# Kernel optimization log

Hardware: AMD Instinct MI355X
Metric: run time of the kernel (lower is better)

Reference implementation:

```python
import jax, jax.numpy as jnp
import numpy as np


def setup_inputs() -> dict:
    key = jax.random.key(0)
    k1, k2 = jax.random.split(key)
    N, D, n_bags, per_bag = 8192, 512, 64, 128
    features = jax.random.normal(k1, (N, D), dtype=jnp.float32)
    # sorted bag indicator: 64 bags x 128 instances each
    batch = jnp.repeat(jnp.arange(n_bags, dtype=jnp.int32), per_bag)
    W = jax.random.normal(k2, (D, D), dtype=jnp.float32) * np.float32(1.0 / np.sqrt(D))
    b = jnp.zeros((D,), dtype=jnp.float32)
    return {"features": features, "W": W, "b": b, "batch": batch, "n_topk": 16, "n_bags": n_bags}


def reference(features, W, b, batch, n_topk, n_bags):
    N = features.shape[0]
    # F.normalize(dim=1): x / max(||x||, eps)
    norm = jnp.sqrt(jnp.sum(features * features, axis=1, keepdims=True))
    nf = features / jnp.maximum(norm, 1e-12)
    corr = nf @ nf.T  # [N, N] cosine-similarity map
    same_bag = batch[:, None] == batch[None, :]
    adj = jnp.where(same_bag, corr, 0.0)
    # scatter-zero the (N - n_topk) smallest per row == keep n_topk largest per row
    _, top_idx = jax.lax.top_k(adj, n_topk)  # [N, n_topk]
    keep = jnp.zeros((N, N), dtype=bool).at[jnp.arange(N)[:, None], top_idx].set(True)
    adj = jnp.where(keep, adj, 0.0)
    # dense_to_sparse()[0] keeps only indices -> unit edge weights for GCNConv.
    # GCNConv (gcn_norm, add_self_loops=True): A_hat = binarized adjacency with diag forced to 1.
    eye = jnp.eye(N, dtype=bool)
    A = jnp.where(eye, 1.0, (adj != 0).astype(features.dtype))  # [N, N]
    deg = jnp.sum(A, axis=0)  # degree scattered on target (col) index in PyG
    dis = jax.lax.rsqrt(deg)  # deg >= 1 thanks to self loops
    xw = features @ W  # [N, D]
    # out[col] = d[col]^-1/2 * sum_row A[row,col] * d[row]^-1/2 * xw[row]
    gcn_out = dis[:, None] * (A.T @ (dis[:, None] * xw)) + b
    # one-hot^T @ features == per-bag segment sum
    agg = jax.ops.segment_sum(gcn_out, batch, num_segments=n_bags)  # [n_bags, D]
    return agg, adj
```

## Files before the change

kernel.cpp:

```cpp
#include <hip/hip_runtime.h>
#include <hip/hip_bf16.h>

#define N 8192
#define D 512
#define NBAGS 64
#define PER_BAG 128
#define TOPK 16

typedef float vfloat4 __attribute__((ext_vector_type(4)));

#define WS_INVN   0
#define WS_KIDX   32768
#define WS_KCNT   557056
#define WS_DEG    589824
#define WS_FW     622592

__global__ void norm_kernel(const float* __restrict__ feat,
                            float* __restrict__ invn,
                            int* __restrict__ deg) {
    int t = threadIdx.x;
    if (blockIdx.x < 32) deg[blockIdx.x * 256 + t] = 0;
    int lane = t & 63, w = t >> 6;
    int r = blockIdx.x * 4 + w;
    const float4* fr = (const float4*)(feat + (size_t)r * D);
    float4 a = fr[lane];
    float4 bq = fr[lane + 64];
    float ss = a.x * a.x + a.y * a.y + a.z * a.z + a.w * a.w
             + bq.x * bq.x + bq.y * bq.y + bq.z * bq.z + bq.w * bq.w;
    #pragma unroll
    for (int off = 32; off > 0; off >>= 1) ss += __shfl_down(ss, off);
    if (lane == 0) invn[r] = 1.0f / fmaxf(sqrtf(ss), 1e-12f);
}

__global__ __launch_bounds__(256, 4) void simtopk_kernel(
        const float* __restrict__ feat,
        const float* __restrict__ invn,
        float* __restrict__ adjOut,
        int* __restrict__ keptIdx,
        int* __restrict__ keptCnt,
        int* __restrict__ deg) {
    int rg = blockIdx.x;
    int bag = blockIdx.y;
    int t = threadIdx.x;
    __shared__ float colT[2][32][132];
    __shared__ float rowT[2][32][12];
    int bagBase = bag * PER_BAG;
    int rowBase = bagBase + rg * 8;
    int tx = t & 31;
    int ty = t >> 5;
    float4 acc = make_float4(0.f, 0.f, 0.f, 0.f);

    int kk = t & 31;
    int sub = t >> 5;
    int winHalf = bag >> 5;
    int jw = (bag & 31) >> 3;
    int winLo = (bag & 31) * 32, winHi = winLo + 32;
    vfloat4 zf4 = {0.f, 0.f, 0.f, 0.f};

    #pragma unroll
    for (int c0 = 0; c0 < 16; ++c0)
        colT[0][kk][sub * 16 + c0] =
            feat[(size_t)(bagBase + sub * 16 + c0) * D + kk];
    rowT[0][kk][sub] = feat[(size_t)(rowBase + sub) * D + kk];
    __syncthreads();

    float pf[16], pr;
    for (int it = 0; it < 16; ++it) {
        int cur = it & 1;
        if (it < 15) {
            int k0 = (it + 1) * 32;
            #pragma unroll
            for (int c0 = 0; c0 < 16; ++c0)
                pf[c0] = feat[(size_t)(bagBase + sub * 16 + c0) * D + k0 + kk];
            pr = feat[(size_t)(rowBase + sub) * D + k0 + kk];
        }
        {
            int zr = it >> 1, half = it & 1;
            vfloat4* rowp = (vfloat4*)(adjOut + (size_t)(rowBase + zr) * N)
                            + half * 1024;
            bool hasWin = (half == winHalf);
            #pragma unroll
            for (int j = 0; j < 4; ++j) {
                int f = t + 256 * j;
                if (hasWin && j == jw) {
                    if (f < winLo || f >= winHi)
                        __builtin_nontemporal_store(zf4, &rowp[f]);
                } else {
                    __builtin_nontemporal_store(zf4, &rowp[f]);
                }
            }
        }
        #pragma unroll
        for (int k = 0; k < 32; ++k) {
            float4 cv = *(const float4*)&colT[cur][k][4 * tx];
            float rv = rowT[cur][k][ty];
            acc.x += rv * cv.x; acc.y += rv * cv.y;
            acc.z += rv * cv.z; acc.w += rv * cv.w;
        }
        if (it < 15) {
            int nxt = cur ^ 1;
            #pragma unroll
            for (int c0 = 0; c0 < 16; ++c0)
                colT[nxt][kk][sub * 16 + c0] = pf[c0];
            rowT[nxt][kk][sub] = pr;
        }
        __syncthreads();
    }
    float ic0 = invn[bagBase + 4 * tx];
    float ic1 = invn[bagBase + 4 * tx + 1];
    float ic2 = invn[bagBase + 4 * tx + 2];
    float ic3 = invn[bagBase + 4 * tx + 3];
    float ir = invn[rowBase + ty];
    acc.x *= ir * ic0; acc.y *= ir * ic1;
    acc.z *= ir * ic2; acc.w *= ir * ic3;

    {
        int r = rowBase + ty;
        float o0 = acc.x, o1 = acc.y, o2 = acc.z, o3 = acc.w;
        float w0 = o0, w1 = o1, w2 = o2, w3 = o3;
        int pm = 0, cnt = 0;
        #pragma unroll 1
        for (int itk = 0; itk < TOPK; ++itk) {
            float bv = w0; int bj = 0;
            if (w1 > bv) { bv = w1; bj = 1; }
            if (w2 > bv) { bv = w2; bj = 2; }
            if (w3 > bv) { bv = w3; bj = 3; }
            int bi = 4 * tx + bj;
            #pragma unroll
            for (int s = 1; s < 32; s <<= 1) {
                float ov = __shfl_xor(bv, s);
                int oi = __shfl_xor(bi, s);
                if (ov > bv || (ov == bv && oi < bi)) { bv = ov; bi = oi; }
            }
            if (bv <= 0.0f) break;
            if (tx == 0) keptIdx[(size_t)r * TOPK + cnt] = bi;
            cnt++;
            if ((bi >> 2) == tx) {
                pm |= 1 << (bi & 3);
                int q = bi & 3;
                if (q == 0) w0 = -1e30f;
                else if (q == 1) w1 = -1e30f;
                else if (q == 2) w2 = -1e30f;
                else w3 = -1e30f;
            }
        }
        if (tx == 0) keptCnt[r] = cnt;
        float4 ov4 = make_float4((pm & 1) ? o0 : 0.0f,
                                 (pm & 2) ? o1 : 0.0f,
                                 (pm & 4) ? o2 : 0.0f,
                                 (pm & 8) ? o3 : 0.0f);
        *(float4*)(adjOut + (size_t)r * N + bagBase + 4 * tx) = ov4;
        if (pm & 1) atomicAdd(&deg[bagBase + 4 * tx], 1);
        if (pm & 2) atomicAdd(&deg[bagBase + 4 * tx + 1], 1);
        if (pm & 4) atomicAdd(&deg[bagBase + 4 * tx + 2], 1);
        if (pm & 8) atomicAdd(&deg[bagBase + 4 * tx + 3], 1);
        int selfCol = rg * 8 + ty;
        if (tx == (selfCol >> 2) && !((pm >> (selfCol & 3)) & 1))
            atomicAdd(&deg[bagBase + selfCol], 1);
    }
}

__global__ void wfw_kernel(const float* __restrict__ feat,
                           const int* __restrict__ keptIdx,
                           const int* __restrict__ keptCnt,
                           const int* __restrict__ deg,
                           float* __restrict__ FW) {
    int bag = blockIdx.x;
    int chunk = blockIdx.y;
    int t = threadIdx.x;
    __shared__ float wsh[PER_BAG];
    int bagBase = bag * PER_BAG;
    {
        int r = bagBase + t;
        int cnt = keptCnt[r];
        float sum = 0.0f;
        bool selfin = false;
        for (int k = 0; k < cnt; ++k) {
            int c = keptIdx[(size_t)r * TOPK + k];
            if (c == t) selfin = true;
            sum += rsqrtf((float)deg[bagBase + c]);
        }
        float disr = rsqrtf((float)deg[r]);
        if (!selfin) sum += disr;
        wsh[t] = disr * sum;
    }
    __syncthreads();
    int d = chunk * 128 + t;
    float acc = 0.0f;
    #pragma unroll 8
    for (int r = 0; r < PER_BAG; ++r)
        acc += wsh[r] * feat[(size_t)(bagBase + r) * D + d];
    FW[bag * D + d] = acc;
}

__global__ void agg_kernel(const float* __restrict__ FW,
                           const float* __restrict__ Wm,
                           const float* __restrict__ b,
                           float* __restrict__ aggOut) {
    int bag = blockIdx.x;
    int chunk = blockIdx.y;
    int t = threadIdx.x;
    __shared__ float fws[D];
    fws[t] = FW[bag * D + t];
    fws[256 + t] = FW[bag * D + 256 + t];
    __syncthreads();
    int d = chunk * 256 + t;
    float acc = 0.0f;
    #pragma unroll 8
    for (int k = 0; k < D; ++k)
        acc += fws[k] * Wm[(size_t)k * D + d];
    aggOut[bag * D + d] = acc + 128.0f * b[d];
}

extern "C" void kernel_launch(void* const* d_in, const int* in_sizes, int n_in,
                              void* d_out, int out_size, void* d_ws, size_t ws_size,
                              hipStream_t stream) {
    const float* feat = (const float*)d_in[0];
    const float* Wm   = (const float*)d_in[1];
    const float* b    = (const float*)d_in[2];

    char* ws = (char*)d_ws;
    float* invn   = (float*)(ws + WS_INVN);
    int* keptIdx  = (int*)(ws + WS_KIDX);
    int* keptCnt  = (int*)(ws + WS_KCNT);
    int* deg      = (int*)(ws + WS_DEG);
    float* FW     = (float*)(ws + WS_FW);

    float* aggOut = (float*)d_out;
    float* adjOut = (float*)d_out + NBAGS * D;

    norm_kernel<<<N / 4, 256, 0, stream>>>(feat, invn, deg);
    simtopk_kernel<<<dim3(16, NBAGS), 256, 0, stream>>>(feat, invn, adjOut,
                                                        keptIdx, keptCnt, deg);
    wfw_kernel<<<dim3(NBAGS, 4), PER_BAG, 0, stream>>>(feat, keptIdx, keptCnt,
                                                       deg, FW);
    agg_kernel<<<dim3(NBAGS, 2), 256, 0, stream>>>(FW, Wm, b, aggOut);
}
```

Baseline: 346.4 us.

## Compute 4 rows per thread in similarity-topk kernel to reuse column tiles

Each block of the similarity/top-k kernel now handles 32 rows of a bag instead of 8. Each thread computes a 4x4 register tile, so every column tile loaded from LDS is reused across four rows, and LDS writes are vectorised to float4. The grid shrinks from 16x64 to 4x64 blocks, which cuts redundant global loads of the bag's column features. In exchange, each block zero-fills four times more of the dense adjacency output, and the lower block count with launch bounds of 1 may reduce occupancy and latency hiding on the store-bound zero-fill.

```diff
diff --git a/kernel.cpp b/kernel.cpp
--- a/kernel.cpp
+++ b/kernel.cpp
@@ -32,7 +32,7 @@
     if (lane == 0) invn[r] = 1.0f / fmaxf(sqrtf(ss), 1e-12f);
 }
 
-__global__ __launch_bounds__(256, 4) void simtopk_kernel(
+__global__ __launch_bounds__(256, 1) void simtopk_kernel(
         const float* __restrict__ feat,
         const float* __restrict__ invn,
         float* __restrict__ adjOut,
@@ -43,28 +43,32 @@
     int bag = blockIdx.y;
     int t = threadIdx.x;
     __shared__ float colT[2][32][132];
-    __shared__ float rowT[2][32][12];
+    __shared__ float rowT[2][32][36];
     int bagBase = bag * PER_BAG;
-    int rowBase = bagBase + rg * 8;
+    int rowBase = bagBase + rg * 32;
     int tx = t & 31;
     int ty = t >> 5;
-    float4 acc = make_float4(0.f, 0.f, 0.f, 0.f);
-
     int kk = t & 31;
     int sub = t >> 5;
-    int winHalf = bag >> 5;
-    int jw = (bag & 31) >> 3;
-    int winLo = (bag & 31) * 32, winHi = winLo + 32;
-    vfloat4 zf4 = {0.f, 0.f, 0.f, 0.f};
+
+    float4 acc[4];
+    #pragma unroll
+    for (int rr = 0; rr < 4; ++rr) acc[rr] = make_float4(0.f, 0.f, 0.f, 0.f);
 
     #pragma unroll
     for (int c0 = 0; c0 < 16; ++c0)
         colT[0][kk][sub * 16 + c0] =
             feat[(size_t)(bagBase + sub * 16 + c0) * D + kk];
-    rowT[0][kk][sub] = feat[(size_t)(rowBase + sub) * D + kk];
+    #pragma unroll
+    for (int j = 0; j < 4; ++j)
+        rowT[0][kk][sub * 4 + j] =
+            feat[(size_t)(rowBase + sub * 4 + j) * D + kk];
     __syncthreads();
 
-    float pf[16], pr;
+    int winLo = bag * 32, winHi = winLo + 32;
+    vfloat4 zf4 = {0.f, 0.f, 0.f, 0.f};
+    float pf[16], prr[4];
+
     for (int it = 0; it < 16; ++it) {
         int cur = it & 1;
         if (it < 15) {
@@ -72,51 +76,60 @@
             #pragma unroll
             for (int c0 = 0; c0 < 16; ++c0)
                 pf[c0] = feat[(size_t)(bagBase + sub * 16 + c0) * D + k0 + kk];
-            pr = feat[(size_t)(rowBase + sub) * D + k0 + kk];
-        }
-        {
-            int zr = it >> 1, half = it & 1;
-            vfloat4* rowp = (vfloat4*)(adjOut + (size_t)(rowBase + zr) * N)
-                            + half * 1024;
-            bool hasWin = (half == winHalf);
-            #pragma unroll
-            for (int j = 0; j < 4; ++j) {
+            #pragma unroll
+            for (int j = 0; j < 4; ++j)
+                prr[j] = feat[(size_t)(rowBase + sub * 4 + j) * D + k0 + kk];
+        }
+        #pragma unroll
+        for (int zr = 0; zr < 2; ++zr) {
+            vfloat4* rowp =
+                (vfloat4*)(adjOut + (size_t)(rowBase + 2 * it + zr) * N);
+            #pragma unroll
+            for (int j = 0; j < 8; ++j) {
                 int f = t + 256 * j;
-                if (hasWin && j == jw) {
-                    if (f < winLo || f >= winHi)
-                        __builtin_nontemporal_store(zf4, &rowp[f]);
-                } else {
+                if (f < winLo || f >= winHi)
                     __builtin_nontemporal_store(zf4, &rowp[f]);
-                }
             }
         }
         #pragma unroll
         for (int k = 0; k < 32; ++k) {
             float4 cv = *(const float4*)&colT[cur][k][4 * tx];
-            float rv = rowT[cur][k][ty];
-            acc.x += rv * cv.x; acc.y += rv * cv.y;
-            acc.z += rv * cv.z; acc.w += rv * cv.w;
+            float4 rv = *(const float4*)&rowT[cur][k][4 * ty];
+            acc[0].x += rv.x * cv.x; acc[0].y += rv.x * cv.y;
+            acc[0].z += rv.x * cv.z; acc[0].w += rv.x * cv.w;
+            acc[1].x += rv.y * cv.x; acc[1].y += rv.y * cv.y;
+            acc[1].z += rv.y * cv.z; acc[1].w += rv.y * cv.w;
+            acc[2].x += rv.z * cv.x; acc[2].y += rv.z * cv.y;
+            acc[2].z += rv.z * cv.z; acc[2].w += rv.z * cv.w;
+            acc[3].x += rv.w * cv.x; acc[3].y += rv.w * cv.y;
+            acc[3].z += rv.w * cv.z; acc[3].w += rv.w * cv.w;
         }
         if (it < 15) {
             int nxt = cur ^ 1;
             #pragma unroll
-            for (int c0 = 0; c0 < 16; ++c0)
-                colT[nxt][kk][sub * 16 + c0] = pf[c0];
-            rowT[nxt][kk][sub] = pr;
+            for (int q = 0; q < 4; ++q)
+                *(float4*)&colT[nxt][kk][sub * 16 + 4 * q] =
+                    make_float4(pf[4 * q], pf[4 * q + 1],
+                                pf[4 * q + 2], pf[4 * q + 3]);
+            *(float4*)&rowT[nxt][kk][sub * 4] =
+                make_float4(prr[0], prr[1], prr[2], prr[3]);
         }
         __syncthreads();
     }
+
     float ic0 = invn[bagBase + 4 * tx];
     float ic1 = invn[bagBase + 4 * tx + 1];
     float ic2 = invn[bagBase + 4 * tx + 2];
     float ic3 = invn[bagBase + 4 * tx + 3];
-    float ir = invn[rowBase + ty];
-    acc.x *= ir * ic0; acc.y *= ir * ic1;
-    acc.z *= ir * ic2; acc.w *= ir * ic3;
-
-    {
-        int r = rowBase + ty;
-        float o0 = acc.x, o1 = acc.y, o2 = acc.z, o3 = acc.w;
+
+    #pragma unroll
+    for (int rr = 0; rr < 4; ++rr) {
+        int r = rowBase + 4 * ty + rr;
+        float ir = invn[r];
+        float o0 = acc[rr].x * ir * ic0;
+        float o1 = acc[rr].y * ir * ic1;
+        float o2 = acc[rr].z * ir * ic2;
+        float o3 = acc[rr].w * ir * ic3;
         float w0 = o0, w1 = o1, w2 = o2, w3 = o3;
         int pm = 0, cnt = 0;
         #pragma unroll 1
@@ -154,7 +167,7 @@
         if (pm & 2) atomicAdd(&deg[bagBase + 4 * tx + 1], 1);
         if (pm & 4) atomicAdd(&deg[bagBase + 4 * tx + 2], 1);
         if (pm & 8) atomicAdd(&deg[bagBase + 4 * tx + 3], 1);
-        int selfCol = rg * 8 + ty;
+        int selfCol = rg * 32 + 4 * ty + rr;
         if (tx == (selfCol >> 2) && !((pm >> (selfCol & 3)) & 1))
             atomicAdd(&deg[bagBase + selfCol], 1);
     }
@@ -230,8 +243,8 @@
     float* adjOut = (float*)d_out + NBAGS * D;
 
     norm_kernel<<<N / 4, 256, 0, stream>>>(feat, invn, deg);
-    simtopk_kernel<<<dim3(16, NBAGS), 256, 0, stream>>>(feat, invn, adjOut,
-                                                        keptIdx, keptCnt, deg);
+    simtopk_kernel<<<dim3(4, NBAGS), 256, 0, stream>>>(feat, invn, adjOut,
+                                                       keptIdx, keptCnt, deg);
     wfw_kernel<<<dim3(NBAGS, 4), PER_BAG, 0, stream>>>(feat, keptIdx, keptCnt,
                                                        deg, FW);
     agg_kernel<<<dim3(NBAGS, 2), 256, 0, stream>>>(FW, Wm, b, aggOut);
```

After: 368.8 us. +6.5%, slower.
